# Optimization experiments

Hardware: AMD Instinct MI355X
Metric: run time of the kernel (lower is better)

Reference implementation:

```python
import jax, jax.numpy as jnp
import numpy as np

B, N, C = 2, 2048, 768
H = 16
D = C // H  # head_dim = 48
SCALE = 1.0 / float(np.sqrt(D))


def setup_inputs() -> dict:
    key = jax.random.key(0)
    ks = jax.random.split(key, 5)
    x = jax.random.normal(ks[0], (B, N, C), dtype=jnp.float32)
    # torch nn.Linear weights are [out, in]; apply as x @ W.T
    qkv_w = jax.random.normal(ks[1], (3 * C, C), dtype=jnp.float32) * 0.02
    qkv_b = jax.random.normal(ks[2], (3 * C,), dtype=jnp.float32) * 0.02
    proj_w = jax.random.normal(ks[3], (C, C), dtype=jnp.float32) * 0.02
    proj_b = jax.random.normal(ks[4], (C,), dtype=jnp.float32) * 0.02
    return {"x": x, "qkv_w": qkv_w, "qkv_b": qkv_b, "proj_w": proj_w, "proj_b": proj_b}


def reference(x, qkv_w, qkv_b, proj_w, proj_b):
    # qkv: (B, N, 3C) -> (3, B, H, N, D)
    qkv = x @ qkv_w.T + qkv_b
    qkv = qkv.reshape(B, N, 3, H, D).transpose(2, 0, 3, 1, 4)
    q, k, v = qkv[0], qkv[1], qkv[2]
    # manual attention: full (B, H, N, N) score matrix, as in the original
    attn = jnp.einsum('bhqd,bhkd->bhqk', q, k) * SCALE
    attn = jax.nn.softmax(attn, axis=-1)
    # attn_drop with p=0.0 (eval / deterministic) is identity
    y = jnp.einsum('bhqk,bhkd->bhqd', attn, v)
    y = y.transpose(0, 2, 1, 3).reshape(B, N, C)
    return y @ proj_w.T + proj_b
```

## Files before the change

### kernel.cpp

```cpp
#include <hip/hip_runtime.h>

typedef short v8s __attribute__((ext_vector_type(8)));
typedef short v4s __attribute__((ext_vector_type(4)));
typedef float v4f __attribute__((ext_vector_type(4)));
typedef unsigned uint2v __attribute__((ext_vector_type(2)));
typedef unsigned short u16;

#define NSEQ 2048
#define CDIM 768
#define NH   16
#define DH   48
#define DP   64
#define MROWS 4096
#define N3C  2304
#define BH   32

#if __has_builtin(__builtin_amdgcn_exp2f)
#define EXP2(x) __builtin_amdgcn_exp2f(x)
#else
#define EXP2(x) exp2f(x)
#endif
#if __has_builtin(__builtin_amdgcn_rcpf)
#define RCP(x) __builtin_amdgcn_rcpf(x)
#else
#define RCP(x) (1.0f/(x))
#endif

__device__ __forceinline__ u16 f2bf(float f){
  unsigned u = __float_as_uint(f);
  u += 0x7FFFu + ((u>>16)&1u);
  return (u16)(u>>16);
}
__device__ __forceinline__ unsigned pkbf(float a, float b){
  unsigned x = __float_as_uint(a), y = __float_as_uint(b);
  x += 0x7FFFu + ((x>>16)&1u);
  y += 0x7FFFu + ((y>>16)&1u);
  return (x>>16) | (y & 0xFFFF0000u);
}

__device__ __forceinline__ void load_lds16(const u16* g, u16* l){
  __builtin_amdgcn_global_load_lds((const __attribute__((address_space(1))) void*)g,
                                   (__attribute__((address_space(3))) void*)l, 16, 0, 0);
}

#define XN8  (MROWS*CDIM/8)
#define WN8  (N3C*CDIM/8)
#define PN8  (CDIM*CDIM/8)
#define CONVB ((XN8+WN8+PN8)/256)
__global__ __launch_bounds__(256) void prep(const float* __restrict__ x, const float* __restrict__ w,
                                            const float* __restrict__ pw, u16* __restrict__ dst,
                                            u16* __restrict__ q, u16* __restrict__ k, u16* __restrict__ v){
  int bid = blockIdx.x;
  if (bid < CONVB){
    int i = bid*256 + threadIdx.x;
    const float* src;
    if (i < XN8)            src = x  + (size_t)i*8;
    else if (i < XN8+WN8)   src = w  + (size_t)(i - XN8)*8;
    else                    src = pw + (size_t)(i - XN8 - WN8)*8;
    v4f f0 = ((const v4f*)src)[0];
    v4f f1 = ((const v4f*)src)[1];
    v8s o;
#pragma unroll
    for (int j = 0; j < 4; j++) ((u16*)&o)[j]   = f2bf(f0[j]);
#pragma unroll
    for (int j = 0; j < 4; j++) ((u16*)&o)[4+j] = f2bf(f1[j]);
    ((v8s*)dst)[i] = o;
  } else {
    int idx = (bid - CONVB)*256 + threadIdx.x;
    v8s z = (v8s){0,0,0,0,0,0,0,0};
    int r = idx >> 1, half = idx & 1;
    *(v8s*)(q + (size_t)r*DP + DH + half*8) = z;
    *(v8s*)(k + (size_t)r*DP + DH + half*8) = z;
  }
}

__global__ __launch_bounds__(256) void qkv_gemm(const u16* __restrict__ x, const u16* __restrict__ w,
                                                const float* __restrict__ bias,
                                                u16* __restrict__ q, u16* __restrict__ k, u16* __restrict__ v){
  __shared__ __align__(16) u16 As[128*32];
  __shared__ __align__(16) u16 Bs[128*32];
  const int wave = threadIdx.x >> 6;
  const int lane = threadIdx.x & 63;
  const int l15  = lane & 15;
  const int quad = lane >> 4;
  const int wm = wave & 1, wn = wave >> 1;
  const int m0 = blockIdx.x*128, n0 = blockIdx.y*128;

  const int srow = lane >> 2;
  const int sg   = (lane & 3) ^ ((lane >> 3) & 3);
  const int sgoff = sg*8;

  v4f acc[4][4];
#pragma unroll
  for (int i = 0; i < 4; i++)
#pragma unroll
    for (int j = 0; j < 4; j++) acc[i][j] = (v4f){0.f,0.f,0.f,0.f};

  const int sig = (l15 >> 1) & 3;

  for (int kt = 0; kt < CDIM/32; kt++){
    const int k0 = kt*32;
    __syncthreads();
#pragma unroll
    for (int j = 0; j < 2; j++){
      int c = wave*2 + j;
      int r = c*16 + srow;
      load_lds16(x + (size_t)(m0 + r)*CDIM + k0 + sgoff, &As[c*512]);
      load_lds16(w + (size_t)(n0 + r)*CDIM + k0 + sgoff, &Bs[c*512]);
    }
    __syncthreads();

    v8s af[4], bf[4];
#pragma unroll
    for (int t = 0; t < 4; t++){
      int ra = wm*64 + t*16 + l15;
      af[t] = *(const v8s*)(&As[ra*32 + ((quad ^ sig)<<3)]);
      int rb = wn*64 + t*16 + l15;
      bf[t] = *(const v8s*)(&Bs[rb*32 + ((quad ^ sig)<<3)]);
    }
#pragma unroll
    for (int ti = 0; ti < 4; ti++)
#pragma unroll
      for (int tj = 0; tj < 4; tj++)
        acc[ti][tj] = __builtin_amdgcn_mfma_f32_16x16x32_bf16(af[ti], bf[tj], acc[ti][tj], 0, 0, 0);
  }

  const float QS = 0.2082540589f;
#pragma unroll
  for (int tj = 0; tj < 4; tj++){
    const int c = n0 + wn*64 + tj*16 + l15;
    const float bv = bias[c];
    const int t = c / CDIM;
    const int rem = c - t*CDIM;
    const int h = rem / DH;
    const int d = rem - h*DH;
#pragma unroll
    for (int ti = 0; ti < 4; ti++){
#pragma unroll
      for (int r = 0; r < 4; r++){
        int m = m0 + wm*64 + ti*16 + quad*4 + r;
        int b_ = m >> 11;
        int n  = m & (NSEQ-1);
        float val = acc[ti][tj][r] + bv;
        if (t == 0) val *= QS;
        u16 o  = f2bf(val);
        int bhn = b_*NH + h;
        if (t == 0)      q[((size_t)bhn*NSEQ + n)*DP + d] = o;
        else if (t == 1) k[((size_t)bhn*NSEQ + n)*DP + d] = o;
        else             v[((size_t)bhn*DP + d)*NSEQ + n] = o;
      }
    }
  }
}

__global__ __launch_bounds__(256) void attn(const u16* __restrict__ q, const u16* __restrict__ k,
                                            const u16* __restrict__ v,
                                            float* __restrict__ oacc, float* __restrict__ lacc){
  __shared__ __align__(16) u16 Kl[64*64];
  __shared__ __align__(16) u16 Vl[48*64];
  __shared__ __align__(16) u16 Pl[4*2*1024];
  const int bh = blockIdx.x;
  const int qt = blockIdx.y;
  const int sp = blockIdx.z;
  const int wave = threadIdx.x >> 6;
  const int lane = threadIdx.x & 63;
  const int l15  = lane & 15;
  const int quad = lane >> 4;
  const int lo3  = l15 & 7;
  const u16* qb = q + (size_t)bh*NSEQ*DP;
  const u16* kb = k + (size_t)bh*NSEQ*DP;
  const u16* vb = v + (size_t)bh*DP*NSEQ;
  const int qm = qt*128 + wave*32;

  v8s qf[2][2];
#pragma unroll
  for (int si = 0; si < 2; si++)
#pragma unroll
    for (int ks = 0; ks < 2; ks++)
      qf[si][ks] = *(const v8s*)(qb + (size_t)(qm + si*16 + l15)*DP + ks*32 + quad*8);

  const short one = (short)0x3F80;
  const v8s vones = (l15 == 0) ? (v8s){one,one,one,one,one,one,one,one}
                               : (v8s){0,0,0,0,0,0,0,0};

  v4f o[2][4];
#pragma unroll
  for (int si = 0; si < 2; si++)
#pragma unroll
    for (int i = 0; i < 4; i++) o[si][i] = (v4f){0.f,0.f,0.f,0.f};

  const int sr  = lane >> 3;
  const int soff = ((lane & 7) ^ (sr & 7)) * 8;
  u16* Plw = Pl + wave*2048;

  for (int kt = sp*16; kt < sp*16 + 16; kt++){
    __syncthreads();
    {
#pragma unroll
      for (int p = 0; p < 2; p++){
        int row = p*32 + wave*8 + sr;
        load_lds16(kb + ((size_t)(kt*64 + row))*DP + soff, &Kl[(p*32 + wave*8)*64]);
      }
      {
        int row = wave*8 + sr;
        load_lds16(vb + (size_t)row*NSEQ + kt*64 + soff, &Vl[(wave*8)*64]);
      }
      if (wave < 2){
        int row = 32 + wave*8 + sr;
        load_lds16(vb + (size_t)row*NSEQ + kt*64 + soff, &Vl[(32 + wave*8)*64]);
      }
    }
    __syncthreads();

#pragma unroll
    for (int si = 0; si < 2; si++){
      v4f s[4];
#pragma unroll
      for (int nt = 0; nt < 4; nt++){
        s[nt] = (v4f){0.f,0.f,0.f,0.f};
#pragma unroll
        for (int ks = 0; ks < 2; ks++){
          int rrow = nt*16 + l15;
          v8s kf = *(const v8s*)(&Kl[rrow*64 + (((ks*4+quad) ^ lo3)<<3)]);
          s[nt] = __builtin_amdgcn_mfma_f32_16x16x32_bf16(kf, qf[si][ks], s[nt], 0, 0, 0);
        }
      }
#pragma unroll
      for (int nt = 0; nt < 4; nt++){
        uint2v pw;
        pw.x = pkbf(EXP2(s[nt][0]), EXP2(s[nt][1]));
        pw.y = pkbf(EXP2(s[nt][2]), EXP2(s[nt][3]));
        int g = nt*2 + (quad>>1);
        *(uint2v*)(&Plw[si*1024 + l15*64 + ((g ^ lo3)<<3) + (quad&1)*4]) = pw;
      }
    }

    v8s pa[2][2];
#pragma unroll
    for (int si = 0; si < 2; si++)
#pragma unroll
      for (int ks = 0; ks < 2; ks++){
        int ga = ks*4 + quad;
        pa[si][ks] = *(const v8s*)(&Plw[si*1024 + l15*64 + ((ga ^ lo3)<<3)]);
      }
#pragma unroll
    for (int dt = 0; dt < 3; dt++){
#pragma unroll
      for (int ks = 0; ks < 2; ks++){
        int row = dt*16 + l15;
        v8s vf = *(const v8s*)(&Vl[row*64 + (((ks*4+quad) ^ lo3)<<3)]);
        o[0][dt] = __builtin_amdgcn_mfma_f32_16x16x32_bf16(pa[0][ks], vf, o[0][dt], 0, 0, 0);
        o[1][dt] = __builtin_amdgcn_mfma_f32_16x16x32_bf16(pa[1][ks], vf, o[1][dt], 0, 0, 0);
      }
    }
#pragma unroll
    for (int ks = 0; ks < 2; ks++){
      o[0][3] = __builtin_amdgcn_mfma_f32_16x16x32_bf16(pa[0][ks], vones, o[0][3], 0, 0, 0);
      o[1][3] = __builtin_amdgcn_mfma_f32_16x16x32_bf16(pa[1][ks], vones, o[1][3], 0, 0, 0);
    }
  }

  const int b_ = bh / NH, h = bh % NH;
  float* oa = oacc + (size_t)sp*MROWS*CDIM;
  float* la = lacc + (size_t)sp*MROWS*NH;
#pragma unroll
  for (int si = 0; si < 2; si++){
#pragma unroll
    for (int r = 0; r < 4; r++){
      int rowg = b_*NSEQ + qm + si*16 + quad*4 + r;
#pragma unroll
      for (int dt = 0; dt < 3; dt++)
        oa[(size_t)rowg*CDIM + h*DH + dt*16 + l15] = o[si][dt][r];
      if (l15 == 0) la[rowg*NH + h] = o[si][3][r];
    }
  }
}

__global__ __launch_bounds__(256) void finalize(const float* __restrict__ oacc,
                                                const float* __restrict__ lacc,
                                                u16* __restrict__ y){
  int i = blockIdx.x*256 + threadIdx.x;
  int rowg = i / 192, c4 = i - rowg*192;
  int c = c4*4, h = c / DH;
  float l = lacc[rowg*NH + h] + lacc[MROWS*NH + rowg*NH + h];
  float inv = RCP(l);
  v4f a = *(const v4f*)(oacc + (size_t)rowg*CDIM + c);
  v4f b = *(const v4f*)(oacc + (size_t)MROWS*CDIM + (size_t)rowg*CDIM + c);
  v4s o4;
#pragma unroll
  for (int j = 0; j < 4; j++) o4[j] = (short)f2bf((a[j] + b[j])*inv);
  *(v4s*)(y + (size_t)rowg*CDIM + c) = o4;
}

__global__ __launch_bounds__(256) void proj_gemm(const u16* __restrict__ y, const u16* __restrict__ w,
                                                 const float* __restrict__ bias, float* __restrict__ out){
  __shared__ __align__(16) u16 As[64*32];
  __shared__ __align__(16) u16 Bs[128*32];
  const int wave = threadIdx.x >> 6;
  const int lane = threadIdx.x & 63;
  const int l15  = lane & 15;
  const int quad = lane >> 4;
  const int wm = wave & 1, wn = wave >> 1;
  const int m0 = blockIdx.x*64, n0 = blockIdx.y*128;

  const int srow = lane >> 2;
  const int sg   = (lane & 3) ^ ((lane >> 3) & 3);
  const int sgoff = sg*8;

  v4f acc[2][4];
#pragma unroll
  for (int i = 0; i < 2; i++)
#pragma unroll
    for (int j = 0; j < 4; j++) acc[i][j] = (v4f){0.f,0.f,0.f,0.f};

  const int sig = (l15 >> 1) & 3;

  for (int kt = 0; kt < CDIM/32; kt++){
    const int k0 = kt*32;
    __syncthreads();
    {
      int rA = wave*16 + srow;
      load_lds16(y + (size_t)(m0 + rA)*CDIM + k0 + sgoff, &As[wave*512]);
#pragma unroll
      for (int j = 0; j < 2; j++){
        int c = wave*2 + j;
        int rB = c*16 + srow;
        load_lds16(w + (size_t)(n0 + rB)*CDIM + k0 + sgoff, &Bs[c*512]);
      }
    }
    __syncthreads();

    v8s af[2], bf[4];
#pragma unroll
    for (int t = 0; t < 2; t++){
      int ra = wm*32 + t*16 + l15;
      af[t] = *(const v8s*)(&As[ra*32 + ((quad ^ sig)<<3)]);
    }
#pragma unroll
    for (int t = 0; t < 4; t++){
      int rb = wn*64 + t*16 + l15;
      bf[t] = *(const v8s*)(&Bs[rb*32 + ((quad ^ sig)<<3)]);
    }
#pragma unroll
    for (int ti = 0; ti < 2; ti++)
#pragma unroll
      for (int tj = 0; tj < 4; tj++)
        acc[ti][tj] = __builtin_amdgcn_mfma_f32_16x16x32_bf16(af[ti], bf[tj], acc[ti][tj], 0, 0, 0);
  }

#pragma unroll
  for (int tj = 0; tj < 4; tj++){
    const int c = n0 + wn*64 + tj*16 + l15;
    const float bv = bias[c];
#pragma unroll
    for (int ti = 0; ti < 2; ti++){
#pragma unroll
      for (int r = 0; r < 4; r++){
        int m = m0 + wm*32 + ti*16 + quad*4 + r;
        out[(size_t)m*CDIM + c] = acc[ti][tj][r] + bv;
      }
    }
  }
}

extern "C" void kernel_launch(void* const* d_in, const int* in_sizes, int n_in,
                              void* d_out, int out_size, void* d_ws, size_t ws_size,
                              hipStream_t stream){
  const float* x      = (const float*)d_in[0];
  const float* qkv_w  = (const float*)d_in[1];
  const float* qkv_b  = (const float*)d_in[2];
  const float* proj_w = (const float*)d_in[3];
  const float* proj_b = (const float*)d_in[4];
  float* out = (float*)d_out;

  u16* xb  = (u16*)d_ws;
  u16* wb  = xb  + (size_t)MROWS*CDIM;
  u16* pwb = wb  + (size_t)N3C*CDIM;
  u16* q   = pwb + (size_t)CDIM*CDIM;
  u16* k   = q + (size_t)BH*NSEQ*DP;
  u16* v   = k + (size_t)BH*NSEQ*DP;
  float* oacc = (float*)(v + (size_t)BH*NSEQ*DP);
  float* lacc = oacc + (size_t)2*MROWS*CDIM;
  u16* y = xb;

  prep<<<dim3(CONVB + 512), dim3(256), 0, stream>>>(x, qkv_w, proj_w, xb, q, k, v);
  qkv_gemm<<<dim3(MROWS/128, N3C/128), dim3(256), 0, stream>>>(xb, wb, qkv_b, q, k, v);
  attn<<<dim3(BH, NSEQ/128, 2), dim3(256), 0, stream>>>(q, k, v, oacc, lacc);
  finalize<<<dim3(MROWS*192/256), dim3(256), 0, stream>>>(oacc, lacc, y);
  proj_gemm<<<dim3(MROWS/64, CDIM/128), dim3(256), 0, stream>>>(y, pwb, proj_b, out);
}
```

Measured before the change: 174.4 us.

## Fuse attention finalize into projection GEMM and share K fragments across query tiles

The separate finalize kernel, which normalized and summed the two split-K attention partials into a bf16 buffer, is removed. The projection GEMM now reads the fp32 partial outputs and row sums directly, normalizes them, converts to bf16 and writes its A tile to LDS itself. This saves one launch and the intermediate write and read, but each of the six column blocks re-reads the fp32 partials, and the A load is now synchronous instead of a direct global-to-LDS load. Separately, the QK^T loop in attention loads each K fragment once and uses it for both query sub-tiles, cutting LDS reads.

New measurement: 177.0 us. No clear change (+1.5%).

```diff
diff --git a/kernel.cpp b/kernel.cpp
--- a/kernel.cpp
+++ b/kernel.cpp
@@ -49,7 +49,7 @@
 #define CONVB ((XN8+WN8+PN8)/256)
 __global__ __launch_bounds__(256) void prep(const float* __restrict__ x, const float* __restrict__ w,
                                             const float* __restrict__ pw, u16* __restrict__ dst,
-                                            u16* __restrict__ q, u16* __restrict__ k, u16* __restrict__ v){
+                                            u16* __restrict__ q, u16* __restrict__ k){
   int bid = blockIdx.x;
   if (bid < CONVB){
     int i = bid*256 + threadIdx.x;
@@ -212,28 +212,28 @@
     }
     __syncthreads();
 
-#pragma unroll
-    for (int si = 0; si < 2; si++){
-      v4f s[4];
-#pragma unroll
-      for (int nt = 0; nt < 4; nt++){
-        s[nt] = (v4f){0.f,0.f,0.f,0.f};
-#pragma unroll
-        for (int ks = 0; ks < 2; ks++){
-          int rrow = nt*16 + l15;
-          v8s kf = *(const v8s*)(&Kl[rrow*64 + (((ks*4+quad) ^ lo3)<<3)]);
-          s[nt] = __builtin_amdgcn_mfma_f32_16x16x32_bf16(kf, qf[si][ks], s[nt], 0, 0, 0);
-        }
-      }
+    v4f s[2][4];
+#pragma unroll
+    for (int nt = 0; nt < 4; nt++){
+      int rrow = nt*16 + l15;
+      v8s kf0 = *(const v8s*)(&Kl[rrow*64 + ((quad ^ lo3)<<3)]);
+      v8s kf1 = *(const v8s*)(&Kl[rrow*64 + (((4+quad) ^ lo3)<<3)]);
+      s[0][nt] = __builtin_amdgcn_mfma_f32_16x16x32_bf16(kf0, qf[0][0], (v4f){0.f,0.f,0.f,0.f}, 0, 0, 0);
+      s[0][nt] = __builtin_amdgcn_mfma_f32_16x16x32_bf16(kf1, qf[0][1], s[0][nt], 0, 0, 0);
+      s[1][nt] = __builtin_amdgcn_mfma_f32_16x16x32_bf16(kf0, qf[1][0], (v4f){0.f,0.f,0.f,0.f}, 0, 0, 0);
+      s[1][nt] = __builtin_amdgcn_mfma_f32_16x16x32_bf16(kf1, qf[1][1], s[1][nt], 0, 0, 0);
+    }
+
+#pragma unroll
+    for (int si = 0; si < 2; si++)
 #pragma unroll
       for (int nt = 0; nt < 4; nt++){
         uint2v pw;
-        pw.x = pkbf(EXP2(s[nt][0]), EXP2(s[nt][1]));
-        pw.y = pkbf(EXP2(s[nt][2]), EXP2(s[nt][3]));
+        pw.x = pkbf(EXP2(s[si][nt][0]), EXP2(s[si][nt][1]));
+        pw.y = pkbf(EXP2(s[si][nt][2]), EXP2(s[si][nt][3]));
         int g = nt*2 + (quad>>1);
         *(uint2v*)(&Plw[si*1024 + l15*64 + ((g ^ lo3)<<3) + (quad&1)*4]) = pw;
       }
-    }
 
     v8s pa[2][2];
 #pragma unroll
@@ -276,23 +276,9 @@
   }
 }
 
-__global__ __launch_bounds__(256) void finalize(const float* __restrict__ oacc,
-                                                const float* __restrict__ lacc,
-                                                u16* __restrict__ y){
-  int i = blockIdx.x*256 + threadIdx.x;
-  int rowg = i / 192, c4 = i - rowg*192;
-  int c = c4*4, h = c / DH;
-  float l = lacc[rowg*NH + h] + lacc[MROWS*NH + rowg*NH + h];
-  float inv = RCP(l);
-  v4f a = *(const v4f*)(oacc + (size_t)rowg*CDIM + c);
-  v4f b = *(const v4f*)(oacc + (size_t)MROWS*CDIM + (size_t)rowg*CDIM + c);
-  v4s o4;
-#pragma unroll
-  for (int j = 0; j < 4; j++) o4[j] = (short)f2bf((a[j] + b[j])*inv);
-  *(v4s*)(y + (size_t)rowg*CDIM + c) = o4;
-}
-
-__global__ __launch_bounds__(256) void proj_gemm(const u16* __restrict__ y, const u16* __restrict__ w,
+__global__ __launch_bounds__(256) void proj_gemm(const float* __restrict__ oacc,
+                                                 const float* __restrict__ lacc,
+                                                 const u16* __restrict__ w,
                                                  const float* __restrict__ bias, float* __restrict__ out){
   __shared__ __align__(16) u16 As[64*32];
   __shared__ __align__(16) u16 Bs[128*32];
@@ -306,6 +292,12 @@
   const int srow = lane >> 2;
   const int sg   = (lane & 3) ^ ((lane >> 3) & 3);
   const int sgoff = sg*8;
+  const int ra  = threadIdx.x >> 2;
+  const int gg  = threadIdx.x & 3;
+  const int pA  = gg ^ ((ra>>1)&3);
+  const int rowg = m0 + ra;
+  const float* oa0 = oacc + (size_t)rowg*CDIM;
+  const float* oa1 = oacc + (size_t)MROWS*CDIM + (size_t)rowg*CDIM;
 
   v4f acc[2][4];
 #pragma unroll
@@ -319,13 +311,25 @@
     const int k0 = kt*32;
     __syncthreads();
     {
-      int rA = wave*16 + srow;
-      load_lds16(y + (size_t)(m0 + rA)*CDIM + k0 + sgoff, &As[wave*512]);
+      int c = k0 + gg*8;
+      unsigned h = (unsigned)c / (unsigned)DH;
+      float l = lacc[rowg*NH + h] + lacc[MROWS*NH + rowg*NH + h];
+      float inv = RCP(l);
+      v4f a0 = *(const v4f*)(oa0 + c);
+      v4f a1 = *(const v4f*)(oa0 + c + 4);
+      v4f b0 = *(const v4f*)(oa1 + c);
+      v4f b1 = *(const v4f*)(oa1 + c + 4);
+      v8s ov;
+#pragma unroll
+      for (int j = 0; j < 4; j++) ((u16*)&ov)[j]   = f2bf((a0[j] + b0[j])*inv);
+#pragma unroll
+      for (int j = 0; j < 4; j++) ((u16*)&ov)[4+j] = f2bf((a1[j] + b1[j])*inv);
+      *(v8s*)(&As[ra*32 + pA*8]) = ov;
 #pragma unroll
       for (int j = 0; j < 2; j++){
-        int c = wave*2 + j;
-        int rB = c*16 + srow;
-        load_lds16(w + (size_t)(n0 + rB)*CDIM + k0 + sgoff, &Bs[c*512]);
+        int cch = wave*2 + j;
+        int rB = cch*16 + srow;
+        load_lds16(w + (size_t)(n0 + rB)*CDIM + k0 + sgoff, &Bs[cch*512]);
       }
     }
     __syncthreads();
@@ -333,8 +337,8 @@
     v8s af[2], bf[4];
 #pragma unroll
     for (int t = 0; t < 2; t++){
-      int ra = wm*32 + t*16 + l15;
-      af[t] = *(const v8s*)(&As[ra*32 + ((quad ^ sig)<<3)]);
+      int rr = wm*32 + t*16 + l15;
+      af[t] = *(const v8s*)(&As[rr*32 + ((quad ^ sig)<<3)]);
     }
 #pragma unroll
     for (int t = 0; t < 4; t++){
@@ -381,11 +385,9 @@
   u16* v   = k + (size_t)BH*NSEQ*DP;
   float* oacc = (float*)(v + (size_t)BH*NSEQ*DP);
   float* lacc = oacc + (size_t)2*MROWS*CDIM;
-  u16* y = xb;
-
-  prep<<<dim3(CONVB + 512), dim3(256), 0, stream>>>(x, qkv_w, proj_w, xb, q, k, v);
+
+  prep<<<dim3(CONVB + 512), dim3(256), 0, stream>>>(x, qkv_w, proj_w, xb, q, k);
   qkv_gemm<<<dim3(MROWS/128, N3C/128), dim3(256), 0, stream>>>(xb, wb, qkv_b, q, k, v);
   attn<<<dim3(BH, NSEQ/128, 2), dim3(256), 0, stream>>>(q, k, v, oacc, lacc);
-  finalize<<<dim3(MROWS*192/256), dim3(256), 0, stream>>>(oacc, lacc, y);
-  proj_gemm<<<dim3(MROWS/64, CDIM/128), dim3(256), 0, stream>>>(y, pwb, proj_b, out);
-}
+  proj_gemm<<<dim3(MROWS/64, CDIM/128), dim3(256), 0, stream>>>(oacc, lacc, pwb, proj_b, out);
+}
```

## Double-buffer K/V tiles in attention and use hardware bf16 packing

Applied to the files above, without the earlier changes.

The attention kernel now keeps two LDS buffers for K and V. It prefetches the next key tile while computing on the current one, which drops one barrier per iteration. The QK^T MFMAs for both query sub-tiles are interleaved so each K fragment read from LDS is reused by both. Softmax probabilities are packed to bf16 with the cvt_pk_bf16_f32 builtin when it is available, instead of integer rounding arithmetic. The cost is extra LDS use that may lower occupancy, and reliance on the async LDS loads finishing before the single barrier.

New measurement: 174.4 us. About the same (-0.0%).

```diff
diff --git a/kernel.cpp b/kernel.cpp
--- a/kernel.cpp
+++ b/kernel.cpp
@@ -31,12 +31,21 @@
   u += 0x7FFFu + ((u>>16)&1u);
   return (u16)(u>>16);
 }
+
+#if __has_builtin(__builtin_amdgcn_cvt_pk_bf16_f32)
+typedef __bf16 bf16x2_t __attribute__((ext_vector_type(2)));
+__device__ __forceinline__ unsigned pkbf(float a, float b){
+  bf16x2_t r = __builtin_amdgcn_cvt_pk_bf16_f32(a, b);
+  return __builtin_bit_cast(unsigned, r);
+}
+#else
 __device__ __forceinline__ unsigned pkbf(float a, float b){
   unsigned x = __float_as_uint(a), y = __float_as_uint(b);
   x += 0x7FFFu + ((x>>16)&1u);
   y += 0x7FFFu + ((y>>16)&1u);
   return (x>>16) | (y & 0xFFFF0000u);
 }
+#endif
 
 __device__ __forceinline__ void load_lds16(const u16* g, u16* l){
   __builtin_amdgcn_global_load_lds((const __attribute__((address_space(1))) void*)g,
@@ -49,7 +58,7 @@
 #define CONVB ((XN8+WN8+PN8)/256)
 __global__ __launch_bounds__(256) void prep(const float* __restrict__ x, const float* __restrict__ w,
                                             const float* __restrict__ pw, u16* __restrict__ dst,
-                                            u16* __restrict__ q, u16* __restrict__ k, u16* __restrict__ v){
+                                            u16* __restrict__ q, u16* __restrict__ k){
   int bid = blockIdx.x;
   if (bid < CONVB){
     int i = bid*256 + threadIdx.x;
@@ -156,8 +165,8 @@
 __global__ __launch_bounds__(256) void attn(const u16* __restrict__ q, const u16* __restrict__ k,
                                             const u16* __restrict__ v,
                                             float* __restrict__ oacc, float* __restrict__ lacc){
-  __shared__ __align__(16) u16 Kl[64*64];
-  __shared__ __align__(16) u16 Vl[48*64];
+  __shared__ __align__(16) u16 Kl[2][64*64];
+  __shared__ __align__(16) u16 Vl[2][48*64];
   __shared__ __align__(16) u16 Pl[4*2*1024];
   const int bh = blockIdx.x;
   const int qt = blockIdx.y;
@@ -193,47 +202,47 @@
   const int soff = ((lane & 7) ^ (sr & 7)) * 8;
   u16* Plw = Pl + wave*2048;
 
-  for (int kt = sp*16; kt < sp*16 + 16; kt++){
+  const int krow0 = wave*8 + sr;
+#define STAGE(kt_, b_) do{                                                              \
+    load_lds16(kb + ((size_t)((kt_)*64 + krow0))*DP + soff,      &Kl[b_][krow0*64]);    \
+    load_lds16(kb + ((size_t)((kt_)*64 + 32 + krow0))*DP + soff, &Kl[b_][(32+krow0)*64]);\
+    load_lds16(vb + (size_t)krow0*NSEQ + (kt_)*64 + soff,        &Vl[b_][krow0*64]);    \
+    if (wave < 2)                                                                       \
+      load_lds16(vb + (size_t)(32+krow0)*NSEQ + (kt_)*64 + soff, &Vl[b_][(32+krow0)*64]);\
+  } while(0)
+
+  STAGE(sp*16, 0);
+
+  for (int i = 0; i < 16; i++){
+    const int buf = i & 1;
     __syncthreads();
-    {
-#pragma unroll
-      for (int p = 0; p < 2; p++){
-        int row = p*32 + wave*8 + sr;
-        load_lds16(kb + ((size_t)(kt*64 + row))*DP + soff, &Kl[(p*32 + wave*8)*64]);
-      }
-      {
-        int row = wave*8 + sr;
-        load_lds16(vb + (size_t)row*NSEQ + kt*64 + soff, &Vl[(wave*8)*64]);
-      }
-      if (wave < 2){
-        int row = 32 + wave*8 + sr;
-        load_lds16(vb + (size_t)row*NSEQ + kt*64 + soff, &Vl[(32 + wave*8)*64]);
-      }
-    }
-    __syncthreads();
-
-#pragma unroll
-    for (int si = 0; si < 2; si++){
-      v4f s[4];
-#pragma unroll
-      for (int nt = 0; nt < 4; nt++){
-        s[nt] = (v4f){0.f,0.f,0.f,0.f};
-#pragma unroll
-        for (int ks = 0; ks < 2; ks++){
-          int rrow = nt*16 + l15;
-          v8s kf = *(const v8s*)(&Kl[rrow*64 + (((ks*4+quad) ^ lo3)<<3)]);
-          s[nt] = __builtin_amdgcn_mfma_f32_16x16x32_bf16(kf, qf[si][ks], s[nt], 0, 0, 0);
-        }
-      }
+    if (i < 15) STAGE(sp*16 + i + 1, buf^1);
+
+    const u16* Klb = &Kl[buf][0];
+    const u16* Vlb = &Vl[buf][0];
+
+    v4f s[2][4];
+#pragma unroll
+    for (int nt = 0; nt < 4; nt++){
+      int rrow = nt*16 + l15;
+      v8s kf0 = *(const v8s*)(&Klb[rrow*64 + ((quad ^ lo3)<<3)]);
+      v8s kf1 = *(const v8s*)(&Klb[rrow*64 + (((4+quad) ^ lo3)<<3)]);
+      s[0][nt] = __builtin_amdgcn_mfma_f32_16x16x32_bf16(kf0, qf[0][0], (v4f){0.f,0.f,0.f,0.f}, 0, 0, 0);
+      s[0][nt] = __builtin_amdgcn_mfma_f32_16x16x32_bf16(kf1, qf[0][1], s[0][nt], 0, 0, 0);
+      s[1][nt] = __builtin_amdgcn_mfma_f32_16x16x32_bf16(kf0, qf[1][0], (v4f){0.f,0.f,0.f,0.f}, 0, 0, 0);
+      s[1][nt] = __builtin_amdgcn_mfma_f32_16x16x32_bf16(kf1, qf[1][1], s[1][nt], 0, 0, 0);
+    }
+
+#pragma unroll
+    for (int si = 0; si < 2; si++)
 #pragma unroll
       for (int nt = 0; nt < 4; nt++){
         uint2v pw;
-        pw.x = pkbf(EXP2(s[nt][0]), EXP2(s[nt][1]));
-        pw.y = pkbf(EXP2(s[nt][2]), EXP2(s[nt][3]));
+        pw.x = pkbf(EXP2(s[si][nt][0]), EXP2(s[si][nt][1]));
+        pw.y = pkbf(EXP2(s[si][nt][2]), EXP2(s[si][nt][3]));
         int g = nt*2 + (quad>>1);
         *(uint2v*)(&Plw[si*1024 + l15*64 + ((g ^ lo3)<<3) + (quad&1)*4]) = pw;
       }
-    }
 
     v8s pa[2][2];
 #pragma unroll
@@ -248,7 +257,7 @@
 #pragma unroll
       for (int ks = 0; ks < 2; ks++){
         int row = dt*16 + l15;
-        v8s vf = *(const v8s*)(&Vl[row*64 + (((ks*4+quad) ^ lo3)<<3)]);
+        v8s vf = *(const v8s*)(&Vlb[row*64 + (((ks*4+quad) ^ lo3)<<3)]);
         o[0][dt] = __builtin_amdgcn_mfma_f32_16x16x32_bf16(pa[0][ks], vf, o[0][dt], 0, 0, 0);
         o[1][dt] = __builtin_amdgcn_mfma_f32_16x16x32_bf16(pa[1][ks], vf, o[1][dt], 0, 0, 0);
       }
@@ -383,7 +392,7 @@
   float* lacc = oacc + (size_t)2*MROWS*CDIM;
   u16* y = xb;
 
-  prep<<<dim3(CONVB + 512), dim3(256), 0, stream>>>(x, qkv_w, proj_w, xb, q, k, v);
+  prep<<<dim3(CONVB + 512), dim3(256), 0, stream>>>(x, qkv_w, proj_w, xb, q, k);
   qkv_gemm<<<dim3(MROWS/128, N3C/128), dim3(256), 0, stream>>>(xb, wb, qkv_b, q, k, v);
   attn<<<dim3(BH, NSEQ/128, 2), dim3(256), 0, stream>>>(q, k, v, oacc, lacc);
   finalize<<<dim3(MROWS*192/256), dim3(256), 0, stream>>>(oacc, lacc, y);
```
